# Kernel optimization log

Measured on AMD Instinct MI355X. Metric: run time of the kernel, lower is better.

Reference implementation:

```python
import jax, jax.numpy as jnp
import numpy as np

N_DIMS = 4          # Euclidean GA with metric [1,1,1,1]
NUM_BLADES = 1 << N_DIMS  # 16 blades
B, N_IN, UNITS = 128, 512, 512


def _cayley_table(n_dims: int) -> np.ndarray:
    """Geometric-product Cayley table C[i,j,k] for Euclidean metric (+1,...,+1).

    Blades are indexed by bitmasks over the n basis vectors; e_A * e_B = sign * e_{A^B},
    where sign counts transpositions in the canonical reordering.
    """
    num = 1 << n_dims
    C = np.zeros((num, num, num), dtype=np.float32)
    for a in range(num):
        for b in range(num):
            t, swaps = a >> 1, 0
            while t:
                swaps += bin(t & b).count("1")
                t >>= 1
            C[a, b, a ^ b] = -1.0 if (swaps & 1) else 1.0
    return C


def setup_inputs() -> dict:
    key = jax.random.key(0)
    k1, k2, k3 = jax.random.split(key, 3)
    x = jax.random.normal(k1, (B, N_IN, NUM_BLADES), dtype=jnp.float32)
    w = jax.random.normal(k2, (UNITS, N_IN, NUM_BLADES), dtype=jnp.float32)
    b = jax.random.normal(k3, (UNITS, NUM_BLADES), dtype=jnp.float32)
    cayley = jnp.asarray(_cayley_table(N_DIMS))
    return {"x": x, "w": w, "b": b, "cayley": cayley}


def reference(x, w, b, cayley):
    # geom_prod(x[..., None, n, i], w[u, n, j])[..., u, n, k], summed over n, plus bias:
    # out[b,u,k] = sum_{n,i,j} x[b,n,i] * cayley[i,j,k] * w[u,n,j] + b[u,k]
    out = jnp.einsum("bni,ijk,unj->buk", x, cayley, w)
    return out + b
```

## Files before the change

### kernel.cpp

```cpp
#include <hip/hip_runtime.h>
#include <stdint.h>

typedef unsigned short ushort_t;
typedef __attribute__((ext_vector_type(8))) short short8v;
typedef __attribute__((ext_vector_type(4))) float f32x4;

#define NSPLIT 4

#define AT_ELEMS (16u * 128u * 512u)
#define WT_ELEMS (16u * 512u * 512u)
#define P_OFF_BYTES ((size_t)(AT_ELEMS + WT_ELEMS) * 2u)
#define P_ELEMS ((size_t)NSPLIT * 16 * 128 * 512)
#define WS_NEEDED (P_OFF_BYTES + P_ELEMS * 4u)

__host__ __device__ constexpr int ga_sign_i(int a, int b) {
  int t = a >> 1, sw = 0;
  while (t) {
    int x = t & b;
    while (x) { sw += x & 1; x >>= 1; }
    t >>= 1;
  }
  return (sw & 1) ? -1 : 1;
}

struct SignTab { int s[16][16]; };
constexpr SignTab make_tab() {
  SignTab t{};
  for (int i = 0; i < 16; i++)
    for (int j = 0; j < 16; j++) t.s[i][j] = ga_sign_i(i, j);
  return t;
}
constexpr SignTab STAB = make_tab();

__device__ __forceinline__ ushort_t f2bf(float f) {
  unsigned u = __float_as_uint(f);
  u = (u + 0x7FFFu + ((u >> 16) & 1u)) >> 16;
  return (ushort_t)u;
}

__device__ __forceinline__ short8v neg_bf16x8(short8v v) {
  const short m = (short)0x8000;
  return v ^ (short8v){m, m, m, m, m, m, m, m};
}

#define PREP_XT (16 * 128 * 64)
#define PREP_TOT (PREP_XT + 16 * 512 * 64)

__global__ __launch_bounds__(256) void prep_kernel(const float* __restrict__ x,
                                                   const float* __restrict__ w,
                                                   ushort_t* __restrict__ At,
                                                   ushort_t* __restrict__ Wt) {
  int tid = blockIdx.x * 256 + threadIdx.x;
  if (tid < PREP_XT) {
    int n8 = tid & 63;
    int bj = tid >> 6;
    int b = bj & 127, j = bj >> 7;
    ushort_t o[8];
#pragma unroll
    for (int r = 0; r < 8; r++)
      o[r] = f2bf(x[((size_t)(b * 512 + n8 * 8 + r)) * 16 + j]);
    *(uint4*)(At + ((size_t)(j * 128 + b)) * 512 + n8 * 8) = *(const uint4*)o;
  } else {
    int t = tid - PREP_XT;
    int n8 = t & 63;
    int uj = t >> 6;
    int u = uj & 511, j = uj >> 9;
    ushort_t o[8];
#pragma unroll
    for (int r = 0; r < 8; r++)
      o[r] = f2bf(w[((size_t)(u * 512 + n8 * 8 + r)) * 16 + j]);
    *(uint4*)(Wt + ((size_t)(j * 512 + u)) * 512 + n8 * 8) = *(const uint4*)o;
  }
}

template <int W>
__device__ __forceinline__ void compute_chunk(const char* sm, int lbx,
                                              f32x4 (&acc)[4][2]) {
#pragma unroll
  for (int jh = 0; jh < 4; jh++) {
    const int ig = jh ^ W;
    short8v av[4], avn[4], bv[4][2];
#pragma unroll
    for (int il = 0; il < 4; il++) {
      av[il] = *(const short8v*)(sm + (ig * 4 + il) * 1024 + lbx);
      avn[il] = neg_bf16x8(av[il]);
    }
#pragma unroll
    for (int jl = 0; jl < 4; jl++)
#pragma unroll
      for (int g = 0; g < 2; g++)
        bv[jl][g] = *(const short8v*)(sm + 16384 + (jh * 4 + jl) * 2048 + g * 1024 + lbx);
#pragma unroll
    for (int kl = 0; kl < 4; kl++) {
#pragma unroll
      for (int jl = 0; jl < 4; jl++) {
        const int il = jl ^ kl;
        const int i = ig * 4 + il;
        const int j = jh * 4 + jl;
        const short8v a = (STAB.s[i][j] < 0) ? avn[il] : av[il];
        acc[kl][0] = __builtin_amdgcn_mfma_f32_16x16x32_bf16(a, bv[jl][0], acc[kl][0], 0, 0, 0);
        acc[kl][1] = __builtin_amdgcn_mfma_f32_16x16x32_bf16(a, bv[jl][1], acc[kl][1], 0, 0, 0);
      }
    }
  }
}

__global__ __launch_bounds__(256, 2) void gemm_kernel(const ushort_t* __restrict__ At,
                                                      const ushort_t* __restrict__ Wt,
                                                      float* __restrict__ P) {
  __shared__ __align__(16) ushort_t smem[24576];

  const int ut = blockIdx.x;
  const int bt = blockIdx.y;
  const int sp = blockIdx.z;
  const int u0 = ut * 32, b0 = bt * 16, n0 = sp * 128;

  const int wv = threadIdx.x >> 6;
  const int lane = threadIdx.x & 63;

  int offX[4], offW[8];
#pragma unroll
  for (int it = 0; it < 4; it++) {
    int slot = it * 256 + wv * 64 + lane;
    int r = slot >> 2, p = slot & 3;
    int q = p ^ (r & 3) ^ ((r >> 2) & 3);
    offX[it] = ((r >> 4) * 128 + (r & 15)) * 512 + q * 8;
  }
#pragma unroll
  for (int it = 0; it < 8; it++) {
    int slot = it * 256 + wv * 64 + lane;
    int r = slot >> 2, p = slot & 3;
    int q = p ^ (r & 3) ^ ((r >> 2) & 3);
    offW[it] = ((r >> 5) * 512 + (r & 31)) * 512 + q * 8;
  }
  const ushort_t* Ax = At + (size_t)b0 * 512 + n0;
  const ushort_t* Wx = Wt + (size_t)u0 * 512 + n0;

  const int la = lane & 15, q = lane >> 4;
  const int lbx = la * 64 + (q ^ (la & 3) ^ ((la >> 2) & 3)) * 16;

  f32x4 acc[4][2];
#pragma unroll
  for (int a = 0; a < 4; a++)
#pragma unroll
    for (int g = 0; g < 2; g++) acc[a][g] = (f32x4){0.f, 0.f, 0.f, 0.f};

  const char* sm = (const char*)smem;

#pragma unroll 1
  for (int kt = 0; kt < 4; kt++) {
#pragma unroll
    for (int it = 0; it < 4; it++)
      __builtin_amdgcn_global_load_lds(
          (const __attribute__((address_space(1))) unsigned int*)(Ax + offX[it] + kt * 32),
          (__attribute__((address_space(3))) unsigned int*)(&smem[(it * 256 + wv * 64) * 8]),
          16, 0, 0);
#pragma unroll
    for (int it = 0; it < 8; it++)
      __builtin_amdgcn_global_load_lds(
          (const __attribute__((address_space(1))) unsigned int*)(Wx + offW[it] + kt * 32),
          (__attribute__((address_space(3))) unsigned int*)(&smem[8192 + (it * 256 + wv * 64) * 8]),
          16, 0, 0);
    __syncthreads();
    switch (wv) {
      case 0: compute_chunk<0>(sm, lbx, acc); break;
      case 1: compute_chunk<1>(sm, lbx, acc); break;
      case 2: compute_chunk<2>(sm, lbx, acc); break;
      default: compute_chunk<3>(sm, lbx, acc); break;
    }
    __syncthreads();
  }

  float* Pb = P + (size_t)sp * 16 * 128 * 512;
#pragma unroll
  for (int kl = 0; kl < 4; kl++) {
    int k = wv * 4 + kl;
#pragma unroll
    for (int g = 0; g < 2; g++)
#pragma unroll
      for (int r2 = 0; r2 < 4; r2++) {
        int row = b0 + q * 4 + r2;
        int col = u0 + g * 16 + la;
        Pb[((size_t)(k * 128 + row)) * 512 + col] = acc[kl][g][r2];
      }
  }
}

__global__ __launch_bounds__(256) void reduce_kernel(const float* __restrict__ P,
                                                     const float* __restrict__ bias,
                                                     float* __restrict__ out) {
  int t = blockIdx.x * 256 + threadIdx.x;
  int u = t & 511;
  int b = t >> 9;
  float acc[16];
#pragma unroll
  for (int k = 0; k < 16; k++) acc[k] = bias[u * 16 + k];
  for (int s = 0; s < NSPLIT; s++) {
#pragma unroll
    for (int k = 0; k < 16; k++)
      acc[k] += P[((size_t)(s * 16 + k) * 128 + b) * 512 + u];
  }
  float* op = out + ((size_t)(b * 512 + u)) * 16;
#pragma unroll
  for (int qq = 0; qq < 4; qq++)
    ((float4*)op)[qq] = make_float4(acc[qq * 4 + 0], acc[qq * 4 + 1],
                                    acc[qq * 4 + 2], acc[qq * 4 + 3]);
}

__global__ __launch_bounds__(256) void naive_kernel(const float* __restrict__ x,
                                                    const float* __restrict__ w,
                                                    const float* __restrict__ bias,
                                                    float* __restrict__ out) {
  int t = blockIdx.x * 256 + threadIdx.x;
  if (t >= 128 * 512 * 16) return;
  int k = t & 15;
  int u = (t >> 4) & 511;
  int b = t >> 13;
  float sgn[16];
#pragma unroll
  for (int i = 0; i < 16; i++) sgn[i] = (float)ga_sign_i(i, i ^ k);
  float acc = bias[u * 16 + k];
  for (int n = 0; n < 512; n++) {
    const float* xp = x + ((size_t)(b * 512 + n)) * 16;
    const float* wp = w + ((size_t)(u * 512 + n)) * 16;
#pragma unroll
    for (int i = 0; i < 16; i++)
      acc += xp[i] * sgn[i] * wp[i ^ k];
  }
  out[t] = acc;
}

extern "C" void kernel_launch(void* const* d_in, const int* in_sizes, int n_in,
                              void* d_out, int out_size, void* d_ws, size_t ws_size,
                              hipStream_t stream) {
  const float* x    = (const float*)d_in[0];
  const float* w    = (const float*)d_in[1];
  const float* bias = (const float*)d_in[2];
  float* out = (float*)d_out;

  if (ws_size >= WS_NEEDED && d_ws != nullptr) {
    ushort_t* At = (ushort_t*)d_ws;
    ushort_t* Wt = At + AT_ELEMS;
    float* P = (float*)((char*)d_ws + P_OFF_BYTES);

    prep_kernel<<<PREP_TOT / 256, 256, 0, stream>>>(x, w, At, Wt);
    gemm_kernel<<<dim3(16, 8, NSPLIT), 256, 0, stream>>>(At, Wt, P);
    reduce_kernel<<<256, 256, 0, stream>>>(P, bias, out);
  } else {
    naive_kernel<<<(128 * 512 * 16) / 256, 256, 0, stream>>>(x, w, bias, out);
  }
}
```

Measured before the change: 107.5 us.

## Rework prep to read contiguous blades and retile GEMM to 16-unit tiles

The prep kernel now has each thread read all 16 blades of 8 consecutive n values with float4 loads and write 16 transposed bf16 rows. The old version issued strided scalar loads, one per blade. The GEMM tile shrinks from 32 to 16 units and the split-K factor drops from 4 to 2, so each block runs 8 K-steps instead of 4. This keeps 512 blocks, halves the partial-sum buffer the reduce kernel reads, and lowers LDS use per block. The cost is less B-operand reuse per A load and longer serial loops per block.

New measurement: 104.4 us. 2.9% less time.

```diff
diff --git a/kernel.cpp b/kernel.cpp
--- a/kernel.cpp
+++ b/kernel.cpp
@@ -5,7 +5,7 @@
 typedef __attribute__((ext_vector_type(8))) short short8v;
 typedef __attribute__((ext_vector_type(4))) float f32x4;
 
-#define NSPLIT 4
+#define NSPLIT 2
 
 #define AT_ELEMS (16u * 128u * 512u)
 #define WT_ELEMS (16u * 512u * 512u)
@@ -43,43 +43,47 @@
   return v ^ (short8v){m, m, m, m, m, m, m, m};
 }
 
-#define PREP_XT (16 * 128 * 64)
-#define PREP_TOT (PREP_XT + 16 * 512 * 64)
+#define PREP_XT (128 * 64)
+#define PREP_TOT (PREP_XT + 512 * 64)
 
 __global__ __launch_bounds__(256) void prep_kernel(const float* __restrict__ x,
                                                    const float* __restrict__ w,
                                                    ushort_t* __restrict__ At,
                                                    ushort_t* __restrict__ Wt) {
   int tid = blockIdx.x * 256 + threadIdx.x;
+  const float* src;
+  ushort_t* dst;
+  int row, n8, rows;
   if (tid < PREP_XT) {
-    int n8 = tid & 63;
-    int bj = tid >> 6;
-    int b = bj & 127, j = bj >> 7;
-    ushort_t o[8];
-#pragma unroll
-    for (int r = 0; r < 8; r++)
-      o[r] = f2bf(x[((size_t)(b * 512 + n8 * 8 + r)) * 16 + j]);
-    *(uint4*)(At + ((size_t)(j * 128 + b)) * 512 + n8 * 8) = *(const uint4*)o;
+    n8 = tid & 63; row = tid >> 6; rows = 128;
+    src = x; dst = At;
   } else {
     int t = tid - PREP_XT;
-    int n8 = t & 63;
-    int uj = t >> 6;
-    int u = uj & 511, j = uj >> 9;
-    ushort_t o[8];
-#pragma unroll
-    for (int r = 0; r < 8; r++)
-      o[r] = f2bf(w[((size_t)(u * 512 + n8 * 8 + r)) * 16 + j]);
-    *(uint4*)(Wt + ((size_t)(j * 512 + u)) * 512 + n8 * 8) = *(const uint4*)o;
-  }
+    n8 = t & 63; row = t >> 6; rows = 512;
+    src = w; dst = Wt;
+  }
+  ushort_t o[16][8];
+#pragma unroll
+  for (int r = 0; r < 8; r++) {
+    const float4* p = (const float4*)(src + ((size_t)(row * 512 + n8 * 8 + r)) * 16);
+    float4 v0 = p[0], v1 = p[1], v2 = p[2], v3 = p[3];
+    o[0][r]  = f2bf(v0.x); o[1][r]  = f2bf(v0.y); o[2][r]  = f2bf(v0.z); o[3][r]  = f2bf(v0.w);
+    o[4][r]  = f2bf(v1.x); o[5][r]  = f2bf(v1.y); o[6][r]  = f2bf(v1.z); o[7][r]  = f2bf(v1.w);
+    o[8][r]  = f2bf(v2.x); o[9][r]  = f2bf(v2.y); o[10][r] = f2bf(v2.z); o[11][r] = f2bf(v2.w);
+    o[12][r] = f2bf(v3.x); o[13][r] = f2bf(v3.y); o[14][r] = f2bf(v3.z); o[15][r] = f2bf(v3.w);
+  }
+#pragma unroll
+  for (int j = 0; j < 16; j++)
+    *(uint4*)(dst + ((size_t)(j * rows + row)) * 512 + n8 * 8) = *(const uint4*)o[j];
 }
 
 template <int W>
 __device__ __forceinline__ void compute_chunk(const char* sm, int lbx,
-                                              f32x4 (&acc)[4][2]) {
+                                              f32x4 (&acc)[4]) {
 #pragma unroll
   for (int jh = 0; jh < 4; jh++) {
     const int ig = jh ^ W;
-    short8v av[4], avn[4], bv[4][2];
+    short8v av[4], avn[4], bv[4];
 #pragma unroll
     for (int il = 0; il < 4; il++) {
       av[il] = *(const short8v*)(sm + (ig * 4 + il) * 1024 + lbx);
@@ -87,9 +91,7 @@
     }
 #pragma unroll
     for (int jl = 0; jl < 4; jl++)
-#pragma unroll
-      for (int g = 0; g < 2; g++)
-        bv[jl][g] = *(const short8v*)(sm + 16384 + (jh * 4 + jl) * 2048 + g * 1024 + lbx);
+      bv[jl] = *(const short8v*)(sm + 16384 + (jh * 4 + jl) * 1024 + lbx);
 #pragma unroll
     for (int kl = 0; kl < 4; kl++) {
 #pragma unroll
@@ -98,8 +100,7 @@
         const int i = ig * 4 + il;
         const int j = jh * 4 + jl;
         const short8v a = (STAB.s[i][j] < 0) ? avn[il] : av[il];
-        acc[kl][0] = __builtin_amdgcn_mfma_f32_16x16x32_bf16(a, bv[jl][0], acc[kl][0], 0, 0, 0);
-        acc[kl][1] = __builtin_amdgcn_mfma_f32_16x16x32_bf16(a, bv[jl][1], acc[kl][1], 0, 0, 0);
+        acc[kl] = __builtin_amdgcn_mfma_f32_16x16x32_bf16(a, bv[jl], acc[kl], 0, 0, 0);
       }
     }
   }
@@ -108,30 +109,25 @@
 __global__ __launch_bounds__(256, 2) void gemm_kernel(const ushort_t* __restrict__ At,
                                                       const ushort_t* __restrict__ Wt,
                                                       float* __restrict__ P) {
-  __shared__ __align__(16) ushort_t smem[24576];
+  __shared__ __align__(16) ushort_t smem[16384];
 
   const int ut = blockIdx.x;
   const int bt = blockIdx.y;
   const int sp = blockIdx.z;
-  const int u0 = ut * 32, b0 = bt * 16, n0 = sp * 128;
+  const int u0 = ut * 16, b0 = bt * 16, n0 = sp * 256;
 
   const int wv = threadIdx.x >> 6;
   const int lane = threadIdx.x & 63;
 
-  int offX[4], offW[8];
+  int offX[4], offW[4];
 #pragma unroll
   for (int it = 0; it < 4; it++) {
     int slot = it * 256 + wv * 64 + lane;
     int r = slot >> 2, p = slot & 3;
     int q = p ^ (r & 3) ^ ((r >> 2) & 3);
-    offX[it] = ((r >> 4) * 128 + (r & 15)) * 512 + q * 8;
-  }
-#pragma unroll
-  for (int it = 0; it < 8; it++) {
-    int slot = it * 256 + wv * 64 + lane;
-    int r = slot >> 2, p = slot & 3;
-    int q = p ^ (r & 3) ^ ((r >> 2) & 3);
-    offW[it] = ((r >> 5) * 512 + (r & 31)) * 512 + q * 8;
+    int j = r >> 4, rw = r & 15;
+    offX[it] = (j * 128 + rw) * 512 + q * 8;
+    offW[it] = (j * 512 + rw) * 512 + q * 8;
   }
   const ushort_t* Ax = At + (size_t)b0 * 512 + n0;
   const ushort_t* Wx = Wt + (size_t)u0 * 512 + n0;
@@ -139,16 +135,14 @@
   const int la = lane & 15, q = lane >> 4;
   const int lbx = la * 64 + (q ^ (la & 3) ^ ((la >> 2) & 3)) * 16;
 
-  f32x4 acc[4][2];
-#pragma unroll
-  for (int a = 0; a < 4; a++)
-#pragma unroll
-    for (int g = 0; g < 2; g++) acc[a][g] = (f32x4){0.f, 0.f, 0.f, 0.f};
+  f32x4 acc[4];
+#pragma unroll
+  for (int a = 0; a < 4; a++) acc[a] = (f32x4){0.f, 0.f, 0.f, 0.f};
 
   const char* sm = (const char*)smem;
 
 #pragma unroll 1
-  for (int kt = 0; kt < 4; kt++) {
+  for (int kt = 0; kt < 8; kt++) {
 #pragma unroll
     for (int it = 0; it < 4; it++)
       __builtin_amdgcn_global_load_lds(
@@ -156,7 +150,7 @@
           (__attribute__((address_space(3))) unsigned int*)(&smem[(it * 256 + wv * 64) * 8]),
           16, 0, 0);
 #pragma unroll
-    for (int it = 0; it < 8; it++)
+    for (int it = 0; it < 4; it++)
       __builtin_amdgcn_global_load_lds(
           (const __attribute__((address_space(1))) unsigned int*)(Wx + offW[it] + kt * 32),
           (__attribute__((address_space(3))) unsigned int*)(&smem[8192 + (it * 256 + wv * 64) * 8]),
@@ -176,13 +170,11 @@
   for (int kl = 0; kl < 4; kl++) {
     int k = wv * 4 + kl;
 #pragma unroll
-    for (int g = 0; g < 2; g++)
-#pragma unroll
-      for (int r2 = 0; r2 < 4; r2++) {
-        int row = b0 + q * 4 + r2;
-        int col = u0 + g * 16 + la;
-        Pb[((size_t)(k * 128 + row)) * 512 + col] = acc[kl][g][r2];
-      }
+    for (int r2 = 0; r2 < 4; r2++) {
+      int row = b0 + q * 4 + r2;
+      int col = u0 + la;
+      Pb[((size_t)(k * 128 + row)) * 512 + col] = acc[kl][r2];
+    }
   }
 }
 
@@ -244,7 +236,7 @@
     float* P = (float*)((char*)d_ws + P_OFF_BYTES);
 
     prep_kernel<<<PREP_TOT / 256, 256, 0, stream>>>(x, w, At, Wt);
-    gemm_kernel<<<dim3(16, 8, NSPLIT), 256, 0, stream>>>(At, Wt, P);
+    gemm_kernel<<<dim3(32, 8, NSPLIT), 256, 0, stream>>>(At, Wt, P);
     reduce_kernel<<<256, 256, 0, stream>>>(P, bias, out);
   } else {
     naive_kernel<<<(128 * 512 * 16) / 256, 256, 0, stream>>>(x, w, bias, out);
```
